# Kernel optimization log

Measured on AMD Instinct MI355X. Metric: run time of the kernel, lower is better.

## Reference

```python
import jax, jax.numpy as jnp
import numpy as np

D_MODEL = 1024
NUM_HEADS = 16
D_K = D_MODEL // NUM_HEADS


def setup_inputs() -> dict:
    key = jax.random.key(0)
    ks = jax.random.split(key, 7)
    B, S = 2, 2048
    scale = 1.0 / np.sqrt(D_MODEL)
    return {
        "Q": jax.random.normal(ks[0], (B, S, D_MODEL), dtype=jnp.float32),
        "K": jax.random.normal(ks[1], (B, S, D_MODEL), dtype=jnp.float32),
        "V": jax.random.normal(ks[2], (B, S, D_MODEL), dtype=jnp.float32),
        "W_q": jax.random.normal(ks[3], (D_MODEL, D_MODEL), dtype=jnp.float32) * scale,
        "W_k": jax.random.normal(ks[4], (D_MODEL, D_MODEL), dtype=jnp.float32) * scale,
        "W_v": jax.random.normal(ks[5], (D_MODEL, D_MODEL), dtype=jnp.float32) * scale,
        "W_o": jax.random.normal(ks[6], (D_MODEL, D_MODEL), dtype=jnp.float32) * scale,
    }


def _split_heads(x):
    B, S, _ = x.shape
    return x.reshape(B, S, NUM_HEADS, D_K).transpose(0, 2, 1, 3)  # [B,H,S,Dk]


def reference(Q, K, V, W_q, W_k, W_v, W_o):
    # nn.Linear(bias=False): x @ W.T
    q = _split_heads(Q @ W_q.T)
    k = _split_heads(K @ W_k.T)
    v = _split_heads(V @ W_v.T)
    scores = jnp.einsum("bhqd,bhkd->bhqk", q, k) / jnp.sqrt(jnp.float32(D_K))
    probs = jax.nn.softmax(scores, axis=-1)
    out = jnp.einsum("bhqk,bhkd->bhqd", probs, v)  # [B,H,S,Dk]
    B, H, S, Dk = out.shape
    out = out.transpose(0, 2, 1, 3).reshape(B, S, H * Dk)
    return out @ W_o.T
```

## Files before the change

kernel.cpp:

```cpp
#include <hip/hip_runtime.h>
#include <cstdint>

#define D_MODEL 1024
#define NH 16
#define DK 64
#define SEQ 2048
#define BATCH 2
#define M_TOT (BATCH * SEQ)

typedef __bf16 bf16x8          __attribute__((ext_vector_type(8)));
typedef unsigned short u16x8   __attribute__((ext_vector_type(8)));
typedef float  f32x4           __attribute__((ext_vector_type(4)));

union pun8 { u16x8 u; bf16x8 b; };

__device__ __forceinline__ f32x4 mfma16(bf16x8 a, bf16x8 b, f32x4 c) {
    return __builtin_amdgcn_mfma_f32_16x16x32_bf16(a, b, c, 0, 0, 0);
}

__device__ __forceinline__ unsigned short f2bf(float f) {
    union { float f; uint32_t u; } v; v.f = f;
    uint32_t u = v.u;
    return (unsigned short)((u + 0x7FFFu + ((u >> 16) & 1u)) >> 16);
}

__device__ __forceinline__ unsigned short f2bf_trunc(float f) {
    union { float f; uint32_t u; } v; v.f = f;
    return (unsigned short)(v.u >> 16);
}

__device__ __forceinline__ void gl_lds16(const unsigned short* g, unsigned short* l) {
    __builtin_amdgcn_global_load_lds(
        (const __attribute__((address_space(1))) void*)g,
        (__attribute__((address_space(3))) void*)l, 16, 0, 0);
}

__global__ __launch_bounds__(256) void convert_all_kernel(
    const float* __restrict__ Q,  const float* __restrict__ K,
    const float* __restrict__ V,  const float* __restrict__ Wq,
    const float* __restrict__ Wk, const float* __restrict__ Wv,
    const float* __restrict__ Wo,
    unsigned short* __restrict__ Qb,  unsigned short* __restrict__ Kb,
    unsigned short* __restrict__ Vb,  unsigned short* __restrict__ Wqb,
    unsigned short* __restrict__ Wkb, unsigned short* __restrict__ Wvb,
    unsigned short* __restrict__ Wob)
{
    int bid = blockIdx.x;
    const float* src; unsigned short* dst; int base;
    if (bid < 3 * 2048) {
        int r = bid >> 11;
        src  = (r == 0) ? Q  : (r == 1) ? K  : V;
        dst  = (r == 0) ? Qb : (r == 1) ? Kb : Vb;
        base = (bid & 2047) * 2048;
    } else {
        int u = bid - 3 * 2048;
        int r = u >> 9;
        src  = (r == 0) ? Wq  : (r == 1) ? Wk  : (r == 2) ? Wv  : Wo;
        dst  = (r == 0) ? Wqb : (r == 1) ? Wkb : (r == 2) ? Wvb : Wob;
        base = (u & 511) * 2048;
    }
    int i = base + threadIdx.x * 8;
    float4 a = *(const float4*)(src + i);
    float4 b = *(const float4*)(src + i + 4);
    u16x8 o;
    o[0] = f2bf(a.x); o[1] = f2bf(a.y); o[2] = f2bf(a.z); o[3] = f2bf(a.w);
    o[4] = f2bf(b.x); o[5] = f2bf(b.y); o[6] = f2bf(b.z); o[7] = f2bf(b.w);
    *(u16x8*)(dst + i) = o;
}

__global__ __launch_bounds__(256) void qkv_proj_kernel(
    const unsigned short* __restrict__ Q,
    const unsigned short* __restrict__ K,
    const unsigned short* __restrict__ V,
    const unsigned short* __restrict__ Wq,
    const unsigned short* __restrict__ Wk,
    const unsigned short* __restrict__ Wv,
    unsigned short* __restrict__ qb,
    unsigned short* __restrict__ kb,
    unsigned short* __restrict__ vtb)
{
    const int z = blockIdx.z;
    const unsigned short* A  = (z == 0) ? Q  : (z == 1) ? K  : V;
    const unsigned short* Bt = (z == 0) ? Wq : (z == 1) ? Wk : Wv;

    const int m0 = blockIdx.y * 128;
    const int n0 = blockIdx.x * 128;

    __shared__ __align__(16) unsigned short smem[128 * 136];
    unsigned short* As = smem;
    unsigned short* Bs = smem + 128 * 32;
    unsigned short* Cs = smem;

    const int t    = threadIdx.x;
    const int lane = t & 63;
    const int w    = t >> 6;
    const int l15  = lane & 15;
    const int quad = lane >> 4;
    const int wm   = (w >> 1) * 64;
    const int wn   = (w & 1) * 64;

    f32x4 acc[4][4] = {};

    for (int k0 = 0; k0 < D_MODEL; k0 += 32) {
        __syncthreads();
        #pragma unroll
        for (int i = 0; i < 2; i++) {
            int u   = t + i * 256;
            int row = u >> 2;
            int kc  = (u & 3) * 8;
            gl_lds16(&A [(m0 + row) * D_MODEL + k0 + kc], &As[(i * 256 + w * 64) * 8]);
            gl_lds16(&Bt[(n0 + row) * D_MODEL + k0 + kc], &Bs[(i * 256 + w * 64) * 8]);
        }
        __syncthreads();

        bf16x8 a[4], b[4];
        #pragma unroll
        for (int mi = 0; mi < 4; mi++)
            a[mi] = *(const bf16x8*)(&As[(wm + mi * 16 + l15) * 32 + quad * 8]);
        #pragma unroll
        for (int ni = 0; ni < 4; ni++)
            b[ni] = *(const bf16x8*)(&Bs[(wn + ni * 16 + l15) * 32 + quad * 8]);

        #pragma unroll
        for (int mi = 0; mi < 4; mi++)
            #pragma unroll
            for (int ni = 0; ni < 4; ni++)
                acc[mi][ni] = mfma16(a[mi], b[ni], acc[mi][ni]);
    }

    __syncthreads();
    #pragma unroll
    for (int mi = 0; mi < 4; mi++) {
        #pragma unroll
        for (int ni = 0; ni < 4; ni++) {
            #pragma unroll
            for (int r = 0; r < 4; r++) {
                int rloc = wm + mi * 16 + quad * 4 + r;
                int cloc = wn + ni * 16 + l15;
                int rr = (z == 2) ? cloc : rloc;
                int cc = (z == 2) ? rloc : cloc;
                Cs[rr * 136 + cc] = f2bf(acc[mi][ni][r]);
            }
        }
    }
    __syncthreads();
    #pragma unroll
    for (int i = 0; i < 8; i++) {
        int u    = t + i * 256;
        int rrow = u >> 4;
        int cc8  = (u & 15) * 8;
        u16x8 val = *(const u16x8*)(&Cs[rrow * 136 + cc8]);
        unsigned short* dst;
        if (z < 2) {
            int m = m0 + rrow, n = n0 + cc8;
            int bi = m >> 11, s = m & (SEQ - 1);
            int hh = n >> 6,  d = n & (DK - 1);
            dst = ((z == 0) ? qb : kb) + (((size_t)(bi * NH + hh) * SEQ + s) * DK + d);
        } else {
            int dglob = n0 + rrow;
            int bi = m0 >> 11, s = (m0 & (SEQ - 1)) + cc8;
            int hh = dglob >> 6, d = dglob & (DK - 1);
            dst = vtb + (((size_t)(bi * NH + hh) * DK + d) * SEQ + s);
        }
        *(u16x8*)dst = val;
    }
}

__global__ __launch_bounds__(256) void attn_kernel(
    const unsigned short* __restrict__ qb,
    const unsigned short* __restrict__ kb,
    const unsigned short* __restrict__ vtb,
    unsigned short* __restrict__ ctx)
{
    const int qt = blockIdx.x;
    const int h  = blockIdx.y;
    const int b  = blockIdx.z;

    const int t    = threadIdx.x;
    const int lane = t & 63;
    const int w    = t >> 6;
    const int l15  = lane & 15;
    const int quad = lane >> 4;

    const unsigned short* qh = qb  + ((b * NH + h) * SEQ) * DK;
    const unsigned short* kh = kb  + ((b * NH + h) * SEQ) * DK;
    const unsigned short* vh = vtb + ((b * NH + h) * DK) * SEQ;

    __shared__ __align__(16) unsigned short p_lds[4][32][72];
    __shared__ __align__(16) unsigned short Ks[128 * 72];
    __shared__ __align__(16) unsigned short Vs[64 * 136];

    const int qrow0 = qt * 128 + w * 32;
    bf16x8 qa[2][2];
    #pragma unroll
    for (int m = 0; m < 2; m++)
        #pragma unroll
        for (int kk = 0; kk < 2; kk++)
            qa[m][kk] = *(const bf16x8*)(&qh[(qrow0 + m * 16 + l15) * DK + kk * 32 + quad * 8]);

    pun8 ones_p;
    #pragma unroll
    for (int i = 0; i < 8; i++) ones_p.u[i] = 0x3F80;
    const bf16x8 ones = ones_p.b;

    f32x4 o[2][4] = {};
    f32x4 lacc[2] = {};

    const float c_exp2 = 0.125f * 1.44269504f;

    for (int kt = 0; kt < SEQ / 128; kt++) {
        __syncthreads();
        #pragma unroll
        for (int i = 0; i < 4; i++) {
            int u   = t + i * 256;
            int row = u >> 3;
            int c8  = (u & 7) * 8;
            *(u16x8*)(&Ks[row * 72 + c8]) =
                *(const u16x8*)(&kh[(kt * 128 + row) * DK + c8]);
        }
        #pragma unroll
        for (int i = 0; i < 4; i++) {
            int u   = t + i * 256;
            int row = u >> 4;
            int c8  = (u & 15) * 8;
            *(u16x8*)(&Vs[row * 136 + c8]) =
                *(const u16x8*)(&vh[row * SEQ + kt * 128 + c8]);
        }
        __syncthreads();

        #pragma unroll
        for (int hh = 0; hh < 2; hh++) {
            bf16x8 kf[4][2], vf[4][2];
            #pragma unroll
            for (int nb = 0; nb < 4; nb++) {
                const int krow = hh * 64 + nb * 16 + l15;
                kf[nb][0] = *(const bf16x8*)(&Ks[krow * 72 + quad * 8]);
                kf[nb][1] = *(const bf16x8*)(&Ks[krow * 72 + 32 + quad * 8]);
            }
            #pragma unroll
            for (int db = 0; db < 4; db++) {
                vf[db][0] = *(const bf16x8*)(&Vs[(db * 16 + l15) * 136 + hh * 64 + quad * 8]);
                vf[db][1] = *(const bf16x8*)(&Vs[(db * 16 + l15) * 136 + hh * 64 + 32 + quad * 8]);
            }

            f32x4 sacc[2][4] = {};
            #pragma unroll
            for (int m = 0; m < 2; m++)
                #pragma unroll
                for (int nb = 0; nb < 4; nb++) {
                    sacc[m][nb] = mfma16(qa[m][0], kf[nb][0], sacc[m][nb]);
                    sacc[m][nb] = mfma16(qa[m][1], kf[nb][1], sacc[m][nb]);
                }

            #pragma unroll
            for (int m = 0; m < 2; m++)
                #pragma unroll
                for (int nb = 0; nb < 4; nb++)
                    #pragma unroll
                    for (int r = 0; r < 4; r++) {
                        float p = exp2f(sacc[m][nb][r] * c_exp2);
                        p_lds[w][m * 16 + quad * 4 + r][nb * 16 + l15] = f2bf_trunc(p);
                    }

            asm volatile("" ::: "memory");

            bf16x8 pa[2][2];
            #pragma unroll
            for (int m = 0; m < 2; m++)
                #pragma unroll
                for (int kk = 0; kk < 2; kk++)
                    pa[m][kk] = *(const bf16x8*)(&p_lds[w][m * 16 + l15][kk * 32 + quad * 8]);

            asm volatile("" ::: "memory");

            #pragma unroll
            for (int db = 0; db < 4; db++)
                #pragma unroll
                for (int m = 0; m < 2; m++) {
                    o[m][db] = mfma16(pa[m][0], vf[db][0], o[m][db]);
                    o[m][db] = mfma16(pa[m][1], vf[db][1], o[m][db]);
                }

            #pragma unroll
            for (int m = 0; m < 2; m++) {
                lacc[m] = mfma16(pa[m][0], ones, lacc[m]);
                lacc[m] = mfma16(pa[m][1], ones, lacc[m]);
            }
        }
    }

    #pragma unroll
    for (int m = 0; m < 2; m++) {
        const int srow_base = b * SEQ + qt * 128 + w * 32 + m * 16 + quad * 4;
        #pragma unroll
        for (int db = 0; db < 4; db++)
            #pragma unroll
            for (int r = 0; r < 4; r++) {
                float val = o[m][db][r] / lacc[m][r];
                ctx[(srow_base + r) * D_MODEL + h * DK + db * 16 + l15] = f2bf(val);
            }
    }
}

__global__ __launch_bounds__(256) void out_proj_kernel(
    const unsigned short* __restrict__ A,
    const unsigned short* __restrict__ Bt,
    float* __restrict__ out)
{
    const int m0 = blockIdx.y * 64;
    const int n0 = blockIdx.x * 128;

    __shared__ __align__(16) unsigned short As[64 * 32];
    __shared__ __align__(16) unsigned short Bs[128 * 32];

    const int t    = threadIdx.x;
    const int lane = t & 63;
    const int w    = t >> 6;
    const int l15  = lane & 15;
    const int quad = lane >> 4;
    const int wn   = w * 32;

    f32x4 acc[4][2] = {};

    for (int k0 = 0; k0 < D_MODEL; k0 += 32) {
        __syncthreads();
        {
            int row = t >> 2;
            int kc  = (t & 3) * 8;
            gl_lds16(&A[(m0 + row) * D_MODEL + k0 + kc], &As[(w * 64) * 8]);
        }
        #pragma unroll
        for (int i = 0; i < 2; i++) {
            int u   = t + i * 256;
            int row = u >> 2;
            int kc  = (u & 3) * 8;
            gl_lds16(&Bt[(n0 + row) * D_MODEL + k0 + kc], &Bs[(i * 256 + w * 64) * 8]);
        }
        __syncthreads();

        bf16x8 a[4], bfr[2];
        #pragma unroll
        for (int mi = 0; mi < 4; mi++)
            a[mi] = *(const bf16x8*)(&As[(mi * 16 + l15) * 32 + quad * 8]);
        #pragma unroll
        for (int ni = 0; ni < 2; ni++)
            bfr[ni] = *(const bf16x8*)(&Bs[(wn + ni * 16 + l15) * 32 + quad * 8]);

        #pragma unroll
        for (int mi = 0; mi < 4; mi++)
            #pragma unroll
            for (int ni = 0; ni < 2; ni++)
                acc[mi][ni] = mfma16(a[mi], bfr[ni], acc[mi][ni]);
    }

    #pragma unroll
    for (int mi = 0; mi < 4; mi++) {
        #pragma unroll
        for (int ni = 0; ni < 2; ni++) {
            #pragma unroll
            for (int r = 0; r < 4; r++) {
                int m = m0 + mi * 16 + quad * 4 + r;
                int n = n0 + wn + ni * 16 + l15;
                out[m * D_MODEL + n] = acc[mi][ni][r];
            }
        }
    }
}

extern "C" void kernel_launch(void* const* d_in, const int* in_sizes, int n_in,
                              void* d_out, int out_size, void* d_ws, size_t ws_size,
                              hipStream_t stream) {
    const float* Q  = (const float*)d_in[0];
    const float* K  = (const float*)d_in[1];
    const float* V  = (const float*)d_in[2];
    const float* Wq = (const float*)d_in[3];
    const float* Wk = (const float*)d_in[4];
    const float* Wv = (const float*)d_in[5];
    const float* Wo = (const float*)d_in[6];

    const size_t NQ = (size_t)M_TOT * D_MODEL;
    const size_t NW = (size_t)D_MODEL * D_MODEL;

    unsigned short* Qb  = (unsigned short*)d_ws;
    unsigned short* Kb  = Qb  + NQ;
    unsigned short* Vb  = Kb  + NQ;
    unsigned short* Wqb = Vb  + NQ;
    unsigned short* Wkb = Wqb + NW;
    unsigned short* Wvb = Wkb + NW;
    unsigned short* Wob = Wvb + NW;
    unsigned short* qb  = Wob + NW;
    unsigned short* kbf = qb  + NQ;
    unsigned short* vtb = kbf + NQ;
    unsigned short* ctx = vtb + NQ;
    float* out = (float*)d_out;

    convert_all_kernel<<<3 * 2048 + 4 * 512, 256, 0, stream>>>(
        Q, K, V, Wq, Wk, Wv, Wo, Qb, Kb, Vb, Wqb, Wkb, Wvb, Wob);

    dim3 g1(D_MODEL / 128, M_TOT / 128, 3);
    qkv_proj_kernel<<<g1, 256, 0, stream>>>(Qb, Kb, Vb, Wqb, Wkb, Wvb, qb, kbf, vtb);

    dim3 g2(SEQ / 128, NH, BATCH);
    attn_kernel<<<g2, 256, 0, stream>>>(qb, kbf, vtb, ctx);

    dim3 g3(D_MODEL / 128, M_TOT / 64, 1);
    out_proj_kernel<<<g3, 256, 0, stream>>>(ctx, Wob, out);
}
```

Before: 249.4 us.

## Split attention KV tile across two wave groups with LDS reduction

The attention block grows from 256 to 512 threads. Each group of four waves handles one half of every 128-key tile instead of one wave looping over both halves. Partial outputs and row sums are reduced through LDS at the end. The aim is more waves per CU and more latency hiding on the exp/MFMA chain, at the cost of a larger LDS footprint, an extra reduction step, and half the work per wave relative to the tile loads.

```diff
diff --git a/kernel.cpp b/kernel.cpp
--- a/kernel.cpp
+++ b/kernel.cpp
@@ -166,7 +166,7 @@
     }
 }
 
-__global__ __launch_bounds__(256) void attn_kernel(
+__global__ __launch_bounds__(512, 4) void attn_kernel(
     const unsigned short* __restrict__ qb,
     const unsigned short* __restrict__ kb,
     const unsigned short* __restrict__ vtb,
@@ -179,6 +179,8 @@
     const int t    = threadIdx.x;
     const int lane = t & 63;
     const int w    = t >> 6;
+    const int wq   = w & 3;
+    const int wk   = w >> 2;
     const int l15  = lane & 15;
     const int quad = lane >> 4;
 
@@ -186,11 +188,12 @@
     const unsigned short* kh = kb  + ((b * NH + h) * SEQ) * DK;
     const unsigned short* vh = vtb + ((b * NH + h) * DK) * SEQ;
 
-    __shared__ __align__(16) unsigned short p_lds[4][32][72];
-    __shared__ __align__(16) unsigned short Ks[128 * 72];
-    __shared__ __align__(16) unsigned short Vs[64 * 136];
-
-    const int qrow0 = qt * 128 + w * 32;
+    __shared__ __align__(16) unsigned short smem[8 * 32 * 72 + 128 * 72 + 64 * 136];
+    unsigned short* p_lds = smem;
+    unsigned short* Ks    = smem + 8 * 32 * 72;
+    unsigned short* Vs    = Ks + 128 * 72;
+
+    const int qrow0 = qt * 128 + wq * 32;
     bf16x8 qa[2][2];
     #pragma unroll
     for (int m = 0; m < 2; m++)
@@ -211,16 +214,16 @@
     for (int kt = 0; kt < SEQ / 128; kt++) {
         __syncthreads();
         #pragma unroll
-        for (int i = 0; i < 4; i++) {
-            int u   = t + i * 256;
+        for (int i = 0; i < 2; i++) {
+            int u   = t + i * 512;
             int row = u >> 3;
             int c8  = (u & 7) * 8;
             *(u16x8*)(&Ks[row * 72 + c8]) =
                 *(const u16x8*)(&kh[(kt * 128 + row) * DK + c8]);
         }
         #pragma unroll
-        for (int i = 0; i < 4; i++) {
-            int u   = t + i * 256;
+        for (int i = 0; i < 2; i++) {
+            int u   = t + i * 512;
             int row = u >> 4;
             int c8  = (u & 15) * 8;
             *(u16x8*)(&Vs[row * 136 + c8]) =
@@ -228,77 +231,99 @@
         }
         __syncthreads();
 
-        #pragma unroll
-        for (int hh = 0; hh < 2; hh++) {
-            bf16x8 kf[4][2], vf[4][2];
+        bf16x8 kf[4][2], vf[4][2];
+        #pragma unroll
+        for (int nb = 0; nb < 4; nb++) {
+            const int krow = wk * 64 + nb * 16 + l15;
+            kf[nb][0] = *(const bf16x8*)(&Ks[krow * 72 + quad * 8]);
+            kf[nb][1] = *(const bf16x8*)(&Ks[krow * 72 + 32 + quad * 8]);
+        }
+        #pragma unroll
+        for (int db = 0; db < 4; db++) {
+            vf[db][0] = *(const bf16x8*)(&Vs[(db * 16 + l15) * 136 + wk * 64 + quad * 8]);
+            vf[db][1] = *(const bf16x8*)(&Vs[(db * 16 + l15) * 136 + wk * 64 + 32 + quad * 8]);
+        }
+
+        f32x4 sacc[2][4] = {};
+        #pragma unroll
+        for (int m = 0; m < 2; m++)
             #pragma unroll
             for (int nb = 0; nb < 4; nb++) {
-                const int krow = hh * 64 + nb * 16 + l15;
-                kf[nb][0] = *(const bf16x8*)(&Ks[krow * 72 + quad * 8]);
-                kf[nb][1] = *(const bf16x8*)(&Ks[krow * 72 + 32 + quad * 8]);
+                sacc[m][nb] = mfma16(qa[m][0], kf[nb][0], sacc[m][nb]);
+                sacc[m][nb] = mfma16(qa[m][1], kf[nb][1], sacc[m][nb]);
             }
-            #pragma unroll
-            for (int db = 0; db < 4; db++) {
-                vf[db][0] = *(const bf16x8*)(&Vs[(db * 16 + l15) * 136 + hh * 64 + quad * 8]);
-                vf[db][1] = *(const bf16x8*)(&Vs[(db * 16 + l15) * 136 + hh * 64 + 32 + quad * 8]);
+
+        #pragma unroll
+        for (int m = 0; m < 2; m++)
+            #pragma unroll
+            for (int nb = 0; nb < 4; nb++)
+                #pragma unroll
+                for (int r = 0; r < 4; r++) {
+                    float p = exp2f(sacc[m][nb][r] * c_exp2);
+                    p_lds[(w * 32 + m * 16 + quad * 4 + r) * 72 + nb * 16 + l15] = f2bf_trunc(p);
+                }
+
+        asm volatile("" ::: "memory");
+
+        bf16x8 pa[2][2];
+        #pragma unroll
+        for (int m = 0; m < 2; m++)
+            #pragma unroll
+            for (int kk = 0; kk < 2; kk++)
+                pa[m][kk] = *(const bf16x8*)(&p_lds[(w * 32 + m * 16 + l15) * 72 + kk * 32 + quad * 8]);
+
+        asm volatile("" ::: "memory");
+
+        #pragma unroll
+        for (int db = 0; db < 4; db++)
+            #pragma unroll
+            for (int m = 0; m < 2; m++) {
+                o[m][db] = mfma16(pa[m][0], vf[db][0], o[m][db]);
+                o[m][db] = mfma16(pa[m][1], vf[db][1], o[m][db]);
             }
 
-            f32x4 sacc[2][4] = {};
-            #pragma unroll
-            for (int m = 0; m < 2; m++)
-                #pragma unroll
-                for (int nb = 0; nb < 4; nb++) {
-                    sacc[m][nb] = mfma16(qa[m][0], kf[nb][0], sacc[m][nb]);
-                    sacc[m][nb] = mfma16(qa[m][1], kf[nb][1], sacc[m][nb]);
-                }
-
-            #pragma unroll
-            for (int m = 0; m < 2; m++)
-                #pragma unroll
-                for (int nb = 0; nb < 4; nb++)
-                    #pragma unroll
-                    for (int r = 0; r < 4; r++) {
-                        float p = exp2f(sacc[m][nb][r] * c_exp2);
-                        p_lds[w][m * 16 + quad * 4 + r][nb * 16 + l15] = f2bf_trunc(p);
-                    }
-
-            asm volatile("" ::: "memory");
-
-            bf16x8 pa[2][2];
-            #pragma unroll
-            for (int m = 0; m < 2; m++)
-                #pragma unroll
-                for (int kk = 0; kk < 2; kk++)
-                    pa[m][kk] = *(const bf16x8*)(&p_lds[w][m * 16 + l15][kk * 32 + quad * 8]);
-
-            asm volatile("" ::: "memory");
-
+        #pragma unroll
+        for (int m = 0; m < 2; m++) {
+            lacc[m] = mfma16(pa[m][0], ones, lacc[m]);
+            lacc[m] = mfma16(pa[m][1], ones, lacc[m]);
+        }
+    }
+
+    __syncthreads();
+    float* cbuf = (float*)Ks;
+    float* myq  = cbuf + wq * (32 * 65 + 32);
+    if (wk == 1) {
+        #pragma unroll
+        for (int m = 0; m < 2; m++) {
             #pragma unroll
             for (int db = 0; db < 4; db++)
                 #pragma unroll
-                for (int m = 0; m < 2; m++) {
-                    o[m][db] = mfma16(pa[m][0], vf[db][0], o[m][db]);
-                    o[m][db] = mfma16(pa[m][1], vf[db][1], o[m][db]);
+                for (int r = 0; r < 4; r++)
+                    myq[(m * 16 + quad * 4 + r) * 65 + db * 16 + l15] = o[m][db][r];
+            if (l15 == 0)
+                #pragma unroll
+                for (int r = 0; r < 4; r++)
+                    myq[32 * 65 + m * 16 + quad * 4 + r] = lacc[m][r];
+        }
+    }
+    __syncthreads();
+    if (wk == 0) {
+        #pragma unroll
+        for (int m = 0; m < 2; m++) {
+            const int row_base = m * 16 + quad * 4;
+            float lt[4];
+            #pragma unroll
+            for (int r = 0; r < 4; r++)
+                lt[r] = lacc[m][r] + myq[32 * 65 + row_base + r];
+            const int srow_base = b * SEQ + qt * 128 + wq * 32 + row_base;
+            #pragma unroll
+            for (int db = 0; db < 4; db++)
+                #pragma unroll
+                for (int r = 0; r < 4; r++) {
+                    float val = (o[m][db][r] + myq[(row_base + r) * 65 + db * 16 + l15]) / lt[r];
+                    ctx[(srow_base + r) * D_MODEL + h * DK + db * 16 + l15] = f2bf(val);
                 }
-
-            #pragma unroll
-            for (int m = 0; m < 2; m++) {
-                lacc[m] = mfma16(pa[m][0], ones, lacc[m]);
-                lacc[m] = mfma16(pa[m][1], ones, lacc[m]);
-            }
-        }
-    }
-
-    #pragma unroll
-    for (int m = 0; m < 2; m++) {
-        const int srow_base = b * SEQ + qt * 128 + w * 32 + m * 16 + quad * 4;
-        #pragma unroll
-        for (int db = 0; db < 4; db++)
-            #pragma unroll
-            for (int r = 0; r < 4; r++) {
-                float val = o[m][db][r] / lacc[m][r];
-                ctx[(srow_base + r) * D_MODEL + h * DK + db * 16 + l15] = f2bf(val);
-            }
+        }
     }
 }
 
@@ -401,7 +426,7 @@
     qkv_proj_kernel<<<g1, 256, 0, stream>>>(Qb, Kb, Vb, Wqb, Wkb, Wvb, qb, kbf, vtb);
 
     dim3 g2(SEQ / 128, NH, BATCH);
-    attn_kernel<<<g2, 256, 0, stream>>>(qb, kbf, vtb, ctx);
+    attn_kernel<<<g2, 512, 0, stream>>>(qb, kbf, vtb, ctx);
 
     dim3 g3(D_MODEL / 128, M_TOT / 64, 1);
     out_proj_kernel<<<g3, 256, 0, stream>>>(ctx, Wob, out);
```

Result: slower. 275.9 us (+10.6%).
